# Performance work log

Measured on AMD Instinct MI355X. Metric: run time of the kernel, lower is better.

Reference implementation:

```python
import jax, jax.numpy as jnp
import numpy as np

V_THRESHOLD = 0.5
V_RESET = 0.0
TAU = 5.0
ALPHA = 0.1
BETA = 0.5
SURROGATE_PARAM = 2.0

# Heaviside spike with sigmoid surrogate gradient (ActFun.apply equivalent)
@jax.custom_vjp
def spike_fn(x):
    return (x > 0).astype(x.dtype)

def _spike_fwd(x):
    return spike_fn(x), x

def _spike_bwd(x, g):
    s = jax.nn.sigmoid(SURROGATE_PARAM * x)
    return (g * SURROGATE_PARAM * s * (1.0 - s),)

spike_fn.defvjp(_spike_fwd, _spike_bwd)


def setup_inputs() -> dict:
    key = jax.random.key(0)
    B, T, N = 32, 64, 32768
    X = jax.random.normal(key, (B, T, N), dtype=jnp.float32)
    return {"X": X}


def reference(X):
    # X: [B, T, N]; sequential LIF recurrence over T with cache term
    init = jnp.zeros_like(X[:, 0])  # mem and cache start at 0

    def step(carry, x_t):
        mem, cache = carry
        mem = mem / TAU + (1.0 + ALPHA * cache) * x_t
        spike = spike_fn(mem - V_THRESHOLD)
        mem = (1.0 - spike) * mem + V_RESET * spike  # hard reset (v_reset=0.0)
        cache = BETA * cache + (1.0 - spike)
        return (mem, cache), spike

    X_t = jnp.moveaxis(X, 1, 0)  # [T, B, N]
    _, spikes = jax.lax.scan(step, (init, init), X_t)
    return jnp.moveaxis(spikes, 0, 1)  # [B, T, N]
```

## Files before the change

kernel.cpp:

```cpp
#include <hip/hip_runtime.h>


constexpr int B = 32;
constexpr int T = 64;
constexpr int N = 32768;
constexpr int N2 = N / 2;
constexpr int NTHREADS = B * N2;

__global__ __launch_bounds__(256) void lif_kernel(const float2* __restrict__ X,
                                                  float2* __restrict__ out) {
#pragma clang fp contract(off)
    const int i = blockIdx.x * blockDim.x + threadIdx.x;
    const int b = i >> 14;
    const int n2 = i & (N2 - 1);
    const int base = b * (T * N2) + n2;

    float mem0 = 0.f, mem1 = 0.f;
    float ca0 = 0.f, ca1 = 0.f;

    float2 x0 = X[base];
    float2 x1 = X[base + N2];

    for (int t = 0; t < T; ++t) {
        const float2 xv = x0;
        x0 = x1;
        const int tp2 = (t + 2 < T) ? (t + 2) : (T - 1);
        x1 = X[base + tp2 * N2];

        float2 sv;
        {
            float m = mem0 / 5.0f + (1.0f + 0.1f * ca0) * xv.x;
            float s = ((m - 0.5f) > 0.0f) ? 1.0f : 0.0f;
            mem0 = (1.0f - s) * m;
            ca0 = 0.5f * ca0 + (1.0f - s);
            sv.x = s;
        }
        {
            float m = mem1 / 5.0f + (1.0f + 0.1f * ca1) * xv.y;
            float s = ((m - 0.5f) > 0.0f) ? 1.0f : 0.0f;
            mem1 = (1.0f - s) * m;
            ca1 = 0.5f * ca1 + (1.0f - s);
            sv.y = s;
        }

        out[base + t * N2] = sv;
    }
}

extern "C" void kernel_launch(void* const* d_in, const int* in_sizes, int n_in,
                              void* d_out, int out_size, void* d_ws, size_t ws_size,
                              hipStream_t stream) {
    const float2* X = (const float2*)d_in[0];
    float2* out = (float2*)d_out;
    const int block = 256;
    const int grid = NTHREADS / block;
    lif_kernel<<<grid, block, 0, stream>>>(X, out);
}
```

Measured before the change: 441.3 us.

## Use 128-bit vector loads, deeper prefetch, and nontemporal stores in LIF kernel

New measurement: 498.5 us. 12.9% more time.

```diff
diff --git a/kernel.cpp b/kernel.cpp
--- a/kernel.cpp
+++ b/kernel.cpp
@@ -1,57 +1,71 @@
 #include <hip/hip_runtime.h>
 
+
+typedef float f32x4 __attribute__((ext_vector_type(4)));
 
 constexpr int B = 32;
 constexpr int T = 64;
 constexpr int N = 32768;
-constexpr int N2 = N / 2;
-constexpr int NTHREADS = B * N2;
+constexpr int N4 = N / 4;
+constexpr int NTHREADS = B * N4;
 
-__global__ __launch_bounds__(256) void lif_kernel(const float2* __restrict__ X,
-                                                  float2* __restrict__ out) {
+__global__ __launch_bounds__(256) void lif_kernel(const f32x4* __restrict__ X,
+                                                  f32x4* __restrict__ out) {
 #pragma clang fp contract(off)
     const int i = blockIdx.x * blockDim.x + threadIdx.x;
-    const int b = i >> 14;
-    const int n2 = i & (N2 - 1);
-    const int base = b * (T * N2) + n2;
+    const int b = i >> 13;
+    const int n4 = i & (N4 - 1);
+    const int base = b * (T * N4) + n4;
 
-    float mem0 = 0.f, mem1 = 0.f;
-    float ca0 = 0.f, ca1 = 0.f;
+    const f32x4* __restrict__ Xp = X + base;
+    f32x4* __restrict__ Op = out + base;
 
-    float2 x0 = X[base];
-    float2 x1 = X[base + N2];
+    float mx = 0.f, my = 0.f, mz = 0.f, mw = 0.f;
+    float cx = 0.f, cy = 0.f, cz = 0.f, cw = 0.f;
 
-    for (int t = 0; t < T; ++t) {
-        const float2 xv = x0;
-        x0 = x1;
-        const int tp2 = (t + 2 < T) ? (t + 2) : (T - 1);
-        x1 = X[base + tp2 * N2];
+    f32x4 xa = Xp[0 * N4];
+    f32x4 xb = Xp[1 * N4];
+    f32x4 xc = Xp[2 * N4];
+    f32x4 xd = Xp[3 * N4];
 
-        float2 sv;
-        {
-            float m = mem0 / 5.0f + (1.0f + 0.1f * ca0) * xv.x;
-            float s = ((m - 0.5f) > 0.0f) ? 1.0f : 0.0f;
-            mem0 = (1.0f - s) * m;
-            ca0 = 0.5f * ca0 + (1.0f - s);
-            sv.x = s;
-        }
-        {
-            float m = mem1 / 5.0f + (1.0f + 0.1f * ca1) * xv.y;
-            float s = ((m - 0.5f) > 0.0f) ? 1.0f : 0.0f;
-            mem1 = (1.0f - s) * m;
-            ca1 = 0.5f * ca1 + (1.0f - s);
-            sv.y = s;
-        }
+#define LIF1(mem, ca, xin, sout)                              \
+    {                                                         \
+        float m_ = mem / 5.0f + (1.0f + 0.1f * ca) * (xin);   \
+        float s_ = ((m_ - 0.5f) > 0.0f) ? 1.0f : 0.0f;        \
+        mem = (1.0f - s_) * m_;                               \
+        ca = 0.5f * ca + (1.0f - s_);                         \
+        sout = s_;                                            \
+    }
 
-        out[base + t * N2] = sv;
+#define SUBSTEP(xreg, j)                                      \
+    {                                                         \
+        const f32x4 xv_ = xreg;                               \
+        int tp_ = t + 4 + (j);                                \
+        tp_ = (tp_ < T) ? tp_ : (T - 1);                      \
+        xreg = Xp[tp_ * N4];                                  \
+        f32x4 sv_;                                            \
+        LIF1(mx, cx, xv_.x, sv_.x);                           \
+        LIF1(my, cy, xv_.y, sv_.y);                           \
+        LIF1(mz, cz, xv_.z, sv_.z);                           \
+        LIF1(mw, cw, xv_.w, sv_.w);                           \
+        __builtin_nontemporal_store(sv_, Op + (t + (j)) * N4);\
     }
+
+    for (int t = 0; t < T; t += 4) {
+        SUBSTEP(xa, 0)
+        SUBSTEP(xb, 1)
+        SUBSTEP(xc, 2)
+        SUBSTEP(xd, 3)
+    }
+#undef SUBSTEP
+#undef LIF1
 }
 
 extern "C" void kernel_launch(void* const* d_in, const int* in_sizes, int n_in,
                               void* d_out, int out_size, void* d_ws, size_t ws_size,
                               hipStream_t stream) {
-    const float2* X = (const float2*)d_in[0];
-    float2* out = (float2*)d_out;
+    const f32x4* X = (const f32x4*)d_in[0];
+    f32x4* out = (f32x4*)d_out;
     const int block = 256;
     const int grid = NTHREADS / block;
     lif_kernel<<<grid, block, 0, stream>>>(X, out);
```

## Preload all timesteps per neuron into registers before the recurrence

Applied to the files above, without the earlier changes.

New measurement: 427.5 us. 3.1% less time.

```diff
diff --git a/kernel.cpp b/kernel.cpp
--- a/kernel.cpp
+++ b/kernel.cpp
@@ -4,54 +4,43 @@
 constexpr int B = 32;
 constexpr int T = 64;
 constexpr int N = 32768;
-constexpr int N2 = N / 2;
-constexpr int NTHREADS = B * N2;
+constexpr int NTHREADS = B * N;
 
-__global__ __launch_bounds__(256) void lif_kernel(const float2* __restrict__ X,
-                                                  float2* __restrict__ out) {
+__global__ __launch_bounds__(256) void lif_kernel(const float* __restrict__ X,
+                                                  float* __restrict__ out) {
 #pragma clang fp contract(off)
     const int i = blockIdx.x * blockDim.x + threadIdx.x;
-    const int b = i >> 14;
-    const int n2 = i & (N2 - 1);
-    const int base = b * (T * N2) + n2;
+    const int b = i >> 15;
+    const int n = i & (N - 1);
+    const int base = b * (T * N) + n;
 
-    float mem0 = 0.f, mem1 = 0.f;
-    float ca0 = 0.f, ca1 = 0.f;
+    const float* __restrict__ Xp = X + base;
+    float* __restrict__ Op = out + base;
 
-    float2 x0 = X[base];
-    float2 x1 = X[base + N2];
+    float xs[T];
+#pragma unroll
+    for (int t = 0; t < T; ++t) {
+        xs[t] = Xp[t * N];
+    }
 
+    __builtin_amdgcn_sched_barrier(0);
+
+    float mem = 0.f, ca = 0.f;
+#pragma unroll
     for (int t = 0; t < T; ++t) {
-        const float2 xv = x0;
-        x0 = x1;
-        const int tp2 = (t + 2 < T) ? (t + 2) : (T - 1);
-        x1 = X[base + tp2 * N2];
-
-        float2 sv;
-        {
-            float m = mem0 / 5.0f + (1.0f + 0.1f * ca0) * xv.x;
-            float s = ((m - 0.5f) > 0.0f) ? 1.0f : 0.0f;
-            mem0 = (1.0f - s) * m;
-            ca0 = 0.5f * ca0 + (1.0f - s);
-            sv.x = s;
-        }
-        {
-            float m = mem1 / 5.0f + (1.0f + 0.1f * ca1) * xv.y;
-            float s = ((m - 0.5f) > 0.0f) ? 1.0f : 0.0f;
-            mem1 = (1.0f - s) * m;
-            ca1 = 0.5f * ca1 + (1.0f - s);
-            sv.y = s;
-        }
-
-        out[base + t * N2] = sv;
+        float m = mem / 5.0f + (1.0f + 0.1f * ca) * xs[t];
+        float s = ((m - 0.5f) > 0.0f) ? 1.0f : 0.0f;
+        mem = (1.0f - s) * m;
+        ca = 0.5f * ca + (1.0f - s);
+        Op[t * N] = s;
     }
 }
 
 extern "C" void kernel_launch(void* const* d_in, const int* in_sizes, int n_in,
                               void* d_out, int out_size, void* d_ws, size_t ws_size,
                               hipStream_t stream) {
-    const float2* X = (const float2*)d_in[0];
-    float2* out = (float2*)d_out;
+    const float* X = (const float*)d_in[0];
+    float* out = (float*)d_out;
     const int block = 256;
     const int grid = NTHREADS / block;
     lif_kernel<<<grid, block, 0, stream>>>(X, out);
```
